# Optimization experiments

Measured on AMD Instinct MI355X. Metric: run time of the kernel, lower is better.

Reference implementation:

```python
import jax, jax.numpy as jnp
import numpy as np

NUM_HEADS = 16
HEAD_SIZE = 64
ROPE_THETA = 10000.0


def _rope_tables(T, dim):
    # freqs_cis equivalent: cos/sin tables of shape [T, dim//2]
    inv_freq = 1.0 / (ROPE_THETA ** (jnp.arange(0, dim, 2, dtype=jnp.float32) / dim))
    angle = jnp.arange(T, dtype=jnp.float32)[:, None] * inv_freq[None, :]  # [T, dim/2]
    return jnp.cos(angle), jnp.sin(angle)


def _apply_rope(x, cos, sin):
    # x: [B, H, T, D]; interleaved pairs rotated by angle (complex multiply)
    x2 = x.reshape(*x.shape[:-1], -1, 2)  # [B,H,T,D/2,2]
    x0, x1 = x2[..., 0], x2[..., 1]
    c = cos[None, None, :, :]
    s = sin[None, None, :, :]
    r0 = x0 * c - x1 * s
    r1 = x0 * s + x1 * c
    return jnp.stack([r0, r1], axis=-1).reshape(x.shape)


def setup_inputs() -> dict:
    key = jax.random.key(0)
    ks = jax.random.split(key, 6)
    B, T, C = 4, 2048, 1024
    scale = 1.0 / np.sqrt(C)
    return {
        "x": jax.random.normal(ks[0], (B, T, C), dtype=jnp.float32),
        "Wq": jax.random.normal(ks[1], (C, C), dtype=jnp.float32) * scale,
        "Wk": jax.random.normal(ks[2], (C, C), dtype=jnp.float32) * scale,
        "Wv": jax.random.normal(ks[3], (C, C), dtype=jnp.float32) * scale,
        "Wo": jax.random.normal(ks[4], (C, C), dtype=jnp.float32) * scale,
        "bo": jax.random.normal(ks[5], (C,), dtype=jnp.float32) * 0.01,
    }


def reference(x, Wq, Wk, Wv, Wo, bo):
    B, T, C = x.shape
    H, D = NUM_HEADS, HEAD_SIZE
    # QKV projections (bias-free), split heads -> [B, H, T, D]
    q = (x @ Wq).reshape(B, T, H, D).transpose(0, 2, 1, 3)
    k = (x @ Wk).reshape(B, T, H, D).transpose(0, 2, 1, 3)
    v = (x @ Wv).reshape(B, T, H, D).transpose(0, 2, 1, 3)
    cos, sin = _rope_tables(T, D)
    q = _apply_rope(q, cos, sin)
    k = _apply_rope(k, cos, sin)
    # causal attention with manual stable softmax
    scores = jnp.einsum("bhqd,bhkd->bhqk", q, k) * (D ** -0.5)
    causal = jnp.tril(jnp.ones((T, T), dtype=bool))
    scores = jnp.where(causal[None, None], scores, -jnp.inf)
    probs = jax.nn.softmax(scores, axis=-1)
    out = jnp.einsum("bhqk,bhkd->bhqd", probs, v)  # [B,H,T,D]
    out = out.transpose(0, 2, 1, 3).reshape(B, T, C)
    return out @ Wo + bo
```

## Files before the change

kernel.cpp:

```cpp
#include <hip/hip_runtime.h>
#include <math.h>

#define HH 16
#define DD 64
#define TT 2048
#define BB 4
#define CC 1024
#define MM (BB*TT)

typedef __attribute__((ext_vector_type(8))) short short8;
typedef __attribute__((ext_vector_type(4))) float f32x4;
typedef __attribute__((ext_vector_type(8))) unsigned short bfu8;
typedef __attribute__((ext_vector_type(4))) unsigned short bfu4;

__device__ __forceinline__ unsigned short f2bf(float f) {
    unsigned int u = __builtin_bit_cast(unsigned int, f);
    unsigned int r = (u + 0x7fffu + ((u >> 16) & 1u)) >> 16;
    return (unsigned short)r;
}
__device__ __forceinline__ float bf2f(unsigned short s) {
    unsigned int u = ((unsigned int)s) << 16;
    return __builtin_bit_cast(float, u);
}

__global__ __launch_bounds__(256) void convert_x(
    const float* __restrict__ x, unsigned short* __restrict__ xb)
{
    const size_t i = (size_t)blockIdx.x * 256 + threadIdx.x;
    const float4 a = ((const float4*)x)[i * 2];
    const float4 b = ((const float4*)x)[i * 2 + 1];
    bfu8 o;
    o[0] = f2bf(a.x); o[1] = f2bf(a.y); o[2] = f2bf(a.z); o[3] = f2bf(a.w);
    o[4] = f2bf(b.x); o[5] = f2bf(b.y); o[6] = f2bf(b.z); o[7] = f2bf(b.w);
    *(bfu8*)(xb + i * 8) = o;
}

__global__ __launch_bounds__(256) void transpose_w(
    const float* __restrict__ Wq, const float* __restrict__ Wk,
    const float* __restrict__ Wv, const float* __restrict__ Wo,
    unsigned short* __restrict__ Wt)
{
    __shared__ float st[64][65];
    const int z = blockIdx.z;
    const float* W = (z == 0) ? Wq : (z == 1) ? Wk : (z == 2) ? Wv : Wo;
    unsigned short* out = Wt + (size_t)z * CC * CC;
    const int rb = blockIdx.y * 64, cb = blockIdx.x * 64;
    const int t = threadIdx.x;
    const int tr = t >> 4, tc4 = (t & 15) * 4;
    #pragma unroll
    for (int i = 0; i < 4; ++i) {
        const int r = i * 16 + tr;
        const float4 v = *(const float4*)&W[(size_t)(rb + r) * CC + cb + tc4];
        st[r][tc4 + 0] = v.x; st[r][tc4 + 1] = v.y;
        st[r][tc4 + 2] = v.z; st[r][tc4 + 3] = v.w;
    }
    __syncthreads();
    #pragma unroll
    for (int i = 0; i < 4; ++i) {
        const int c = i * 16 + tr;
        bfu4 o;
        o[0] = f2bf(st[tc4 + 0][c]); o[1] = f2bf(st[tc4 + 1][c]);
        o[2] = f2bf(st[tc4 + 2][c]); o[3] = f2bf(st[tc4 + 3][c]);
        *(bfu4*)&out[(size_t)(cb + c) * CC + rb + tc4] = o;
    }
}

__global__ __launch_bounds__(256) void rope_tables(float2* __restrict__ tab)
{
    const int i = blockIdx.x * 256 + threadIdx.x;
    const int t = i >> 5, p = i & 31;
    const float inv_freq = expf(-(float)(2 * p) * (9.210340371976184f / 64.0f));
    const float ang = (float)t * inv_freq;
    float s, c;
    sincosf(ang, &s, &c);
    tab[i] = make_float2(c, s);
}

__global__ __launch_bounds__(256) void transpose_v(
    const unsigned short* __restrict__ v, unsigned short* __restrict__ vt)
{
    const int bh = blockIdx.y;
    const int t  = blockIdx.x * 256 + threadIdx.x;
    const unsigned short* src = v + ((size_t)bh * TT + t) * DD;
    #pragma unroll
    for (int d0 = 0; d0 < 64; d0 += 8) {
        const bfu8 x = *(const bfu8*)(src + d0);
        #pragma unroll
        for (int j = 0; j < 8; ++j)
            vt[((size_t)bh * DD + d0 + j) * TT + t] = x[j];
    }
}

template<int MODE>
__global__ __launch_bounds__(256) void gemm_mfma(
    const unsigned short* __restrict__ A,
    const unsigned short* __restrict__ Wt,
    const float* __restrict__ bias,
    const float2* __restrict__ tab,
    void* __restrict__ outv)
{
    __shared__ short lds[128 * 32 * 2];
    short* As = lds;
    short* Bs = lds + 128 * 32;

    const int tid  = threadIdx.x;
    const int lane = tid & 63;
    const int w    = tid >> 6;
    const int wr   = w >> 1, wc = w & 1;
    const int mb   = blockIdx.y * 128, nb = blockIdx.x * 128;
    const int z    = (MODE == 1) ? blockIdx.z : 0;
    const unsigned short* Bmat = Wt + (size_t)z * CC * CC;

    f32x4 acc[4][4] = {};

    for (int k0 = 0; k0 < CC; k0 += 32) {
        __syncthreads();
        #pragma unroll
        for (int t2 = 0; t2 < 2; ++t2) {
            const int ci  = w * 128 + t2 * 64 + lane;
            const int row = ci >> 2, kc = ci & 3;
            const unsigned short* ga = A    + (size_t)(mb + row) * CC + k0 + kc * 8;
            const unsigned short* gb = Bmat + (size_t)(nb + row) * CC + k0 + kc * 8;
            __builtin_amdgcn_global_load_lds(
                (const __attribute__((address_space(1))) unsigned int*)ga,
                (__attribute__((address_space(3))) unsigned int*)(As + (w * 2 + t2) * 512),
                16, 0, 0);
            __builtin_amdgcn_global_load_lds(
                (const __attribute__((address_space(1))) unsigned int*)gb,
                (__attribute__((address_space(3))) unsigned int*)(Bs + (w * 2 + t2) * 512),
                16, 0, 0);
        }
        __syncthreads();

        short8 a[4], b[4];
        #pragma unroll
        for (int i = 0; i < 4; ++i) {
            const int ro = (wr * 64 + i * 16 + (lane & 15)) * 32 + (lane >> 4) * 8;
            a[i] = *(const short8*)&As[ro];
            const int co = (wc * 64 + i * 16 + (lane & 15)) * 32 + (lane >> 4) * 8;
            b[i] = *(const short8*)&Bs[co];
        }
        #pragma unroll
        for (int i = 0; i < 4; ++i)
            #pragma unroll
            for (int j = 0; j < 4; ++j)
                acc[i][j] = __builtin_amdgcn_mfma_f32_16x16x32_bf16(
                    a[i], b[j], acc[i][j], 0, 0, 0);
    }

    if (MODE == 0) {
        float* out = (float*)outv;
        #pragma unroll
        for (int i = 0; i < 4; ++i) {
            const int m0 = mb + wr * 64 + i * 16 + (lane >> 4) * 4;
            #pragma unroll
            for (int j = 0; j < 4; ++j) {
                const int n = nb + wc * 64 + j * 16 + (lane & 15);
                const float bv = bias[n];
                #pragma unroll
                for (int r = 0; r < 4; ++r)
                    out[(size_t)(m0 + r) * CC + n] = acc[i][j][r] + bv;
            }
        }
    } else {
        unsigned short* dst = (unsigned short*)outv + (size_t)z * MM * CC;
        const bool do_rope = (z < 2);
        #pragma unroll
        for (int i = 0; i < 4; ++i) {
            const int m0 = mb + wr * 64 + i * 16 + (lane >> 4) * 4;
            #pragma unroll
            for (int j = 0; j < 4; ++j) {
                const int n = nb + wc * 64 + j * 16 + (lane & 15);
                const int h = n >> 6, d = n & 63;
                #pragma unroll
                for (int r = 0; r < 4; ++r) {
                    const int m  = m0 + r;
                    const int b_ = m >> 11, t = m & (TT - 1);
                    const float val     = acc[i][j][r];
                    const float partner = __shfl_xor(val, 1);
                    float r0, r1;
                    if (do_rope) {
                        const float2 cs = tab[t * 32 + (d >> 1)];
                        r0 = val * cs.x - partner * cs.y;
                        r1 = val * cs.y + partner * cs.x;
                    } else {
                        r0 = val; r1 = partner;
                    }
                    if ((lane & 1) == 0) {
                        const unsigned int pk =
                            (unsigned int)f2bf(r0) | ((unsigned int)f2bf(r1) << 16);
                        *(unsigned int*)&dst[(((size_t)(b_ * HH + h) * TT + t) * DD) + (d & ~1)] = pk;
                    }
                }
            }
        }
    }
}

__global__ __launch_bounds__(256) void attn_mfma(
    const unsigned short* __restrict__ qg, const unsigned short* __restrict__ kg,
    const unsigned short* __restrict__ vtg, unsigned short* __restrict__ att)
{
    __shared__ short Ks[64 * 64];
    __shared__ short Vs[64 * 64];
    __shared__ short Ps[4][16 * 64];

    const int tid  = threadIdx.x;
    const int lane = tid & 63;
    const int w    = tid >> 6;
    const int l15  = lane & 15, l4 = lane >> 4;
    const int qt   = blockIdx.x;
    const int bh   = blockIdx.y;
    const int qb   = qt * 64;
    const int b_   = bh >> 4, h = bh & 15;

    const unsigned short* qrow = qg + ((size_t)bh * TT + qb + w * 16 + l15) * DD;
    const short8 qf0 = *(const short8*)(qrow + l4 * 8);
    const short8 qf1 = *(const short8*)(qrow + 32 + l4 * 8);

    f32x4 acc_o[4] = {};
    float m_run[4] = {-1e30f, -1e30f, -1e30f, -1e30f};
    float l_run[4] = {};

    const int srow = tid >> 2;
    const int sc0  = (tid & 3) * 16;

    const int ntile = qt + 1;
    for (int kt = 0; kt < ntile; ++kt) {
        const int kb = kt * 64;
        __syncthreads();
        #pragma unroll
        for (int half = 0; half < 2; ++half) {
            const int c0 = sc0 + half * 8;
            const short8 kv = *(const short8*)(kg  + ((size_t)bh * TT + kb + srow) * DD + c0);
            const short8 vv = *(const short8*)(vtg + ((size_t)bh * DD + srow) * TT + kb + c0);
            const int bo = (srow * 128 + c0 * 2) ^ ((srow & 7) << 4);
            *(short8*)((char*)Ks + bo) = kv;
            *(short8*)((char*)Vs + bo) = vv;
        }
        __syncthreads();

        f32x4 s4[4];
        #pragma unroll
        for (int kj = 0; kj < 4; ++kj) {
            const int key = kj * 16 + l15;
            const short8 kf0 = *(const short8*)((char*)Ks + ((key * 128 +      l4 * 16) ^ ((key & 7) << 4)));
            const short8 kf1 = *(const short8*)((char*)Ks + ((key * 128 + 64 + l4 * 16) ^ ((key & 7) << 4)));
            f32x4 zz = {};
            zz = __builtin_amdgcn_mfma_f32_16x16x32_bf16(qf0, kf0, zz, 0, 0, 0);
            zz = __builtin_amdgcn_mfma_f32_16x16x32_bf16(qf1, kf1, zz, 0, 0, 0);
            s4[kj] = zz;
        }

        float p[4][4];
        float tmax[4] = {-1e30f, -1e30f, -1e30f, -1e30f};
        const bool diag = (kt == ntile - 1);
        #pragma unroll
        for (int kj = 0; kj < 4; ++kj)
            #pragma unroll
            for (int r = 0; r < 4; ++r) {
                float s = s4[kj][r] * 0.125f;
                if (diag) {
                    const int key_g = kb + kj * 16 + l15;
                    const int q_g   = qb + w * 16 + l4 * 4 + r;
                    if (key_g > q_g) s = -1e30f;
                }
                p[kj][r] = s;
                tmax[r] = fmaxf(tmax[r], s);
            }
        #pragma unroll
        for (int mk = 1; mk < 16; mk <<= 1)
            #pragma unroll
            for (int r = 0; r < 4; ++r)
                tmax[r] = fmaxf(tmax[r], __shfl_xor(tmax[r], mk));

        #pragma unroll
        for (int r = 0; r < 4; ++r) {
            const float mn   = fmaxf(m_run[r], tmax[r]);
            const float corr = __expf(m_run[r] - mn);
            m_run[r] = mn;
            l_run[r] *= corr;
            #pragma unroll
            for (int dj = 0; dj < 4; ++dj) acc_o[dj][r] *= corr;
            float ls = 0.f;
            #pragma unroll
            for (int kj = 0; kj < 4; ++kj) {
                const float e = __expf(p[kj][r] - mn);
                p[kj][r] = e;
                ls += e;
            }
            l_run[r] += ls;
        }

        #pragma unroll
        for (int kj = 0; kj < 4; ++kj)
            #pragma unroll
            for (int r = 0; r < 4; ++r) {
                const int qr  = l4 * 4 + r;
                const int key = kj * 16 + l15;
                const int bo  = (qr * 128 + key * 2) ^ ((qr & 7) << 4);
                *(short*)((char*)&Ps[w][0] + bo) = (short)f2bf(p[kj][r]);
            }

        const short8 pa0 = *(const short8*)((char*)&Ps[w][0] + ((l15 * 128 +      l4 * 16) ^ ((l15 & 7) << 4)));
        const short8 pa1 = *(const short8*)((char*)&Ps[w][0] + ((l15 * 128 + 64 + l4 * 16) ^ ((l15 & 7) << 4)));
        #pragma unroll
        for (int dj = 0; dj < 4; ++dj) {
            const int dr = dj * 16 + l15;
            const short8 vf0 = *(const short8*)((char*)Vs + ((dr * 128 +      l4 * 16) ^ ((dr & 7) << 4)));
            const short8 vf1 = *(const short8*)((char*)Vs + ((dr * 128 + 64 + l4 * 16) ^ ((dr & 7) << 4)));
            acc_o[dj] = __builtin_amdgcn_mfma_f32_16x16x32_bf16(pa0, vf0, acc_o[dj], 0, 0, 0);
            acc_o[dj] = __builtin_amdgcn_mfma_f32_16x16x32_bf16(pa1, vf1, acc_o[dj], 0, 0, 0);
        }
    }

    #pragma unroll
    for (int mk = 1; mk < 16; mk <<= 1)
        #pragma unroll
        for (int r = 0; r < 4; ++r)
            l_run[r] += __shfl_xor(l_run[r], mk);

    #pragma unroll
    for (int r = 0; r < 4; ++r) {
        const float inv = 1.0f / l_run[r];
        const int t = qb + w * 16 + l4 * 4 + r;
        unsigned short* orow = att + ((size_t)(b_ * TT + t)) * CC + h * DD;
        #pragma unroll
        for (int dj = 0; dj < 4; ++dj)
            orow[dj * 16 + l15] = f2bf(acc_o[dj][r] * inv);
    }
}

extern "C" void kernel_launch(void* const* d_in, const int* in_sizes, int n_in,
                              void* d_out, int out_size, void* d_ws, size_t ws_size,
                              hipStream_t stream) {
    const float* x  = (const float*)d_in[0];
    const float* Wq = (const float*)d_in[1];
    const float* Wk = (const float*)d_in[2];
    const float* Wv = (const float*)d_in[3];
    const float* Wo = (const float*)d_in[4];
    const float* bo = (const float*)d_in[5];
    float* out = (float*)d_out;

    char* ws = (char*)d_ws;
    unsigned short* xb  = (unsigned short*)ws;
    unsigned short* aw  = xb;
    unsigned short* wt  = (unsigned short*)(ws + (16ull << 20));
    unsigned short* qkv = (unsigned short*)(ws + (24ull << 20));
    unsigned short* vt  = (unsigned short*)(ws + (72ull << 20));
    float2*         tab = (float2*)       (ws + (88ull << 20));

    convert_x  <<<4096, 256, 0, stream>>>(x, xb);
    transpose_w<<<dim3(16, 16, 4), 256, 0, stream>>>(Wq, Wk, Wv, Wo, wt);
    rope_tables<<<256, 256, 0, stream>>>(tab);

    gemm_mfma<1><<<dim3(8, 64, 3), 256, 0, stream>>>(xb, wt, nullptr, tab, qkv);

    const size_t NEL = (size_t)MM * CC;
    transpose_v<<<dim3(8, 64), 256, 0, stream>>>(qkv + 2 * NEL, vt);

    attn_mfma<<<dim3(32, 64), 256, 0, stream>>>(qkv, qkv + NEL, vt, aw);

    gemm_mfma<0><<<dim3(8, 64), 256, 0, stream>>>(
        aw, wt + 3ull * CC * CC, bo, tab, out);
}
```

Before: 464.3 us.

## Double-buffer K/V tiles with register prefetch and reverse causal tile order

Loads the next K/V tile into registers while the current tile is being computed, then stores it into a second LDS buffer. This cuts the barriers per iteration from two to one and hides global load latency. Query tiles are now processed in reverse order, so the longest causal blocks are scheduled first for better tail balance. MFMA sections are wrapped in s_setprio hints. The cost is twice the K/V LDS space and more live registers, which could lower occupancy.

```diff
diff --git a/kernel.cpp b/kernel.cpp
--- a/kernel.cpp
+++ b/kernel.cpp
@@ -201,15 +201,15 @@
     const unsigned short* __restrict__ qg, const unsigned short* __restrict__ kg,
     const unsigned short* __restrict__ vtg, unsigned short* __restrict__ att)
 {
-    __shared__ short Ks[64 * 64];
-    __shared__ short Vs[64 * 64];
+    __shared__ short Ks[2][64 * 64];
+    __shared__ short Vs[2][64 * 64];
     __shared__ short Ps[4][16 * 64];
 
     const int tid  = threadIdx.x;
     const int lane = tid & 63;
     const int w    = tid >> 6;
     const int l15  = lane & 15, l4 = lane >> 4;
-    const int qt   = blockIdx.x;
+    const int qt   = 31 - blockIdx.x;
     const int bh   = blockIdx.y;
     const int qb   = qt * 64;
     const int b_   = bh >> 4, h = bh & 15;
@@ -224,33 +224,54 @@
 
     const int srow = tid >> 2;
     const int sc0  = (tid & 3) * 16;
+    const int bo0  = (srow * 128 + sc0 * 2)       ^ ((srow & 7) << 4);
+    const int bo1  = (srow * 128 + (sc0 + 8) * 2) ^ ((srow & 7) << 4);
+    const unsigned short* kst = kg  + ((size_t)bh * TT + srow) * DD + sc0;
+    const unsigned short* vst = vtg + ((size_t)bh * DD + srow) * TT + sc0;
 
     const int ntile = qt + 1;
+
+    {
+        const short8 k0 = *(const short8*)(kst);
+        const short8 k1 = *(const short8*)(kst + 8);
+        const short8 v0 = *(const short8*)(vst);
+        const short8 v1 = *(const short8*)(vst + 8);
+        *(short8*)((char*)&Ks[0][0] + bo0) = k0;
+        *(short8*)((char*)&Ks[0][0] + bo1) = k1;
+        *(short8*)((char*)&Vs[0][0] + bo0) = v0;
+        *(short8*)((char*)&Vs[0][0] + bo1) = v1;
+    }
+    __syncthreads();
+
     for (int kt = 0; kt < ntile; ++kt) {
-        const int kb = kt * 64;
-        __syncthreads();
-        #pragma unroll
-        for (int half = 0; half < 2; ++half) {
-            const int c0 = sc0 + half * 8;
-            const short8 kv = *(const short8*)(kg  + ((size_t)bh * TT + kb + srow) * DD + c0);
-            const short8 vv = *(const short8*)(vtg + ((size_t)bh * DD + srow) * TT + kb + c0);
-            const int bo = (srow * 128 + c0 * 2) ^ ((srow & 7) << 4);
-            *(short8*)((char*)Ks + bo) = kv;
-            *(short8*)((char*)Vs + bo) = vv;
-        }
-        __syncthreads();
+        const int kb  = kt * 64;
+        const int cur = kt & 1;
+        const short* Kc = &Ks[cur][0];
+        const short* Vc = &Vs[cur][0];
+
+        short8 nk0, nk1, nv0, nv1;
+        const bool has_next = (kt + 1 < ntile);
+        if (has_next) {
+            const size_t ko = (size_t)(kb + 64) * DD;
+            nk0 = *(const short8*)(kst + ko);
+            nk1 = *(const short8*)(kst + ko + 8);
+            nv0 = *(const short8*)(vst + kb + 64);
+            nv1 = *(const short8*)(vst + kb + 64 + 8);
+        }
 
         f32x4 s4[4];
+        __builtin_amdgcn_s_setprio(1);
         #pragma unroll
         for (int kj = 0; kj < 4; ++kj) {
             const int key = kj * 16 + l15;
-            const short8 kf0 = *(const short8*)((char*)Ks + ((key * 128 +      l4 * 16) ^ ((key & 7) << 4)));
-            const short8 kf1 = *(const short8*)((char*)Ks + ((key * 128 + 64 + l4 * 16) ^ ((key & 7) << 4)));
+            const short8 kf0 = *(const short8*)((char*)Kc + ((key * 128 +      l4 * 16) ^ ((key & 7) << 4)));
+            const short8 kf1 = *(const short8*)((char*)Kc + ((key * 128 + 64 + l4 * 16) ^ ((key & 7) << 4)));
             f32x4 zz = {};
             zz = __builtin_amdgcn_mfma_f32_16x16x32_bf16(qf0, kf0, zz, 0, 0, 0);
             zz = __builtin_amdgcn_mfma_f32_16x16x32_bf16(qf1, kf1, zz, 0, 0, 0);
             s4[kj] = zz;
         }
+        __builtin_amdgcn_s_setprio(0);
 
         float p[4][4];
         float tmax[4] = {-1e30f, -1e30f, -1e30f, -1e30f};
@@ -304,14 +325,26 @@
 
         const short8 pa0 = *(const short8*)((char*)&Ps[w][0] + ((l15 * 128 +      l4 * 16) ^ ((l15 & 7) << 4)));
         const short8 pa1 = *(const short8*)((char*)&Ps[w][0] + ((l15 * 128 + 64 + l4 * 16) ^ ((l15 & 7) << 4)));
+        __builtin_amdgcn_s_setprio(1);
         #pragma unroll
         for (int dj = 0; dj < 4; ++dj) {
             const int dr = dj * 16 + l15;
-            const short8 vf0 = *(const short8*)((char*)Vs + ((dr * 128 +      l4 * 16) ^ ((dr & 7) << 4)));
-            const short8 vf1 = *(const short8*)((char*)Vs + ((dr * 128 + 64 + l4 * 16) ^ ((dr & 7) << 4)));
+            const short8 vf0 = *(const short8*)((char*)Vc + ((dr * 128 +      l4 * 16) ^ ((dr & 7) << 4)));
+            const short8 vf1 = *(const short8*)((char*)Vc + ((dr * 128 + 64 + l4 * 16) ^ ((dr & 7) << 4)));
             acc_o[dj] = __builtin_amdgcn_mfma_f32_16x16x32_bf16(pa0, vf0, acc_o[dj], 0, 0, 0);
             acc_o[dj] = __builtin_amdgcn_mfma_f32_16x16x32_bf16(pa1, vf1, acc_o[dj], 0, 0, 0);
         }
+        __builtin_amdgcn_s_setprio(0);
+
+        if (has_next) {
+            char* Kn = (char*)&Ks[cur ^ 1][0];
+            char* Vn = (char*)&Vs[cur ^ 1][0];
+            *(short8*)(Kn + bo0) = nk0;
+            *(short8*)(Kn + bo1) = nk1;
+            *(short8*)(Vn + bo0) = nv0;
+            *(short8*)(Vn + bo1) = nv1;
+        }
+        __syncthreads();
     }
 
     #pragma unroll
```

Result: faster. 426.2 us (-8.2%).
